# Performance work log

Measured on AMD Instinct MI355X. Metric: run time of the kernel, lower is better.

The kernel has to match this reference:

```python
import jax, jax.numpy as jnp
import numpy as np


def setup_inputs() -> dict:
    key = jax.random.key(0)
    k0, k1, k2, k3, k4, k5 = jax.random.split(key, 6)
    N, E, F, D, H = 50000, 1000000, 128, 32, 4
    # xavier_normal with gain = calculate_gain('relu') = sqrt(2)
    std = np.sqrt(2.0) * np.sqrt(2.0 / (F + D))
    return {
        "entity_features": jax.random.normal(k0, (N, 1, F), jnp.float32),
        "relation_features": jax.random.normal(k1, (E, 1, F), jnp.float32),
        "src": jax.random.randint(k2, (E,), 0, N, jnp.int32),
        "dst": jax.random.randint(k3, (E,), 0, N, jnp.int32),
        "w_q": jax.random.normal(k4, (H, F, D), jnp.float32) * std,
        "w_k": jax.random.normal(k5, (H, F, D), jnp.float32) * std,
    }


def reference(entity_features, relation_features, src, dst, w_q, w_k):
    # entity_features: (N, 1, F) -> repeat over heads is just a broadcast
    feat = entity_features[:, 0, :]        # (N, F)
    rel = relation_features[:, 0, :]       # (E, F)
    num_heads = w_q.shape[0]
    N = feat.shape[0]

    # per-head projections: q = feat @ w_q, k = feat @ w_k, erel = rel @ w_k
    q = jnp.einsum("nf,hfd->nhd", feat, w_q)      # (N, H, D)  'out_el'
    k = jnp.einsum("nf,hfd->nhd", feat, w_k)      # (N, H, D)  'out_er'
    erel = jnp.einsum("ef,hfd->ehd", rel, w_k)    # (E, H, D)  'out_erel'

    # v_dot_u: dst's out_er . src's out_el ; e_dot_u: edge out_erel . src's out_er
    e = (jnp.einsum("ehd,ehd->eh", k[dst], q[src])
         + jnp.einsum("ehd,ehd->eh", erel, k[src]))   # (E, H)
    e = jax.nn.leaky_relu(e, negative_slope=0.01)

    # edge_softmax normalized by source node (softmax over outgoing edges)
    m = jax.ops.segment_max(e, src, num_segments=N)   # (N, H)
    m = jnp.where(jnp.isfinite(m), m, jnp.zeros_like(m))
    ex = jnp.exp(e - m[src])                          # (E, H)
    denom = jax.ops.segment_sum(ex, src, num_segments=N)  # (N, H)
    att = ex / denom[src]                             # (E, H)

    # squeeze(-1).sum(-1)/num_heads on the (E, H, 1) edge tensor -> mean over heads
    return att.sum(axis=-1) / num_heads               # (E,)
```

## Files before the change

kernel.cpp:

```cpp
#include <hip/hip_runtime.h>

#define HH 4
#define FF 128
#define DD 32

typedef float f32x4 __attribute__((ext_vector_type(4)));


__global__ void scatter_kernel(const int* __restrict__ src, const int* __restrict__ dst,
                               int* __restrict__ cursor, int2* __restrict__ ed, int E) {
    int i = blockIdx.x * blockDim.x + threadIdx.x;
    if (i >= E) return;
    int s = src[i];
    int pos = atomicAdd(&cursor[s], 1);
    long long pack = (unsigned)i | ((long long)dst[i] << 32);
    __builtin_nontemporal_store(pack, (long long*)&ed[pos]);
}


__global__ __launch_bounds__(256) void qk_hist_kernel(
    const float* __restrict__ feat, const float* __restrict__ wq,
    const float* __restrict__ wk, float* __restrict__ q,
    float* __restrict__ k, int N,
    const int* __restrict__ src, int* __restrict__ counts, int E, int QKB) {
    __shared__ float fs[32 * FF];
    int bid = blockIdx.x;
    if (bid >= QKB) {
        int i = ((bid - QKB) * 256 + threadIdx.x) * 4;
        if (i + 3 < E) {
            int4 v = *(const int4*)(src + i);
            atomicAdd(&counts[v.x], 1);
            atomicAdd(&counts[v.y], 1);
            atomicAdd(&counts[v.z], 1);
            atomicAdd(&counts[v.w], 1);
        } else {
            for (; i < E; ++i) atomicAdd(&counts[src[i]], 1);
        }
        return;
    }
    int n0 = bid * 32;
    int nb = N - n0; if (nb > 32) nb = 32;
    const float4* s4 = (const float4*)(feat + (size_t)n0 * FF);
    int nf4 = nb * FF / 4;
    for (int i = threadIdx.x; i < nf4; i += 256) ((float4*)fs)[i] = s4[i];
    __syncthreads();

    int half = threadIdx.x >> 7;
    int o    = threadIdx.x & 127;
    int h = o >> 5, d = o & 31;
    const float* wqp = wq + ((size_t)h * FF) * DD + d;
    const float* wkp = wk + ((size_t)h * FF) * DD + d;

    float accq[16], acck[16];
#pragma unroll
    for (int e = 0; e < 16; ++e) { accq[e] = 0.f; acck[e] = 0.f; }
    for (int f = 0; f < FF; f += 4) {
        float wq0 = wqp[(f + 0) * DD], wq1 = wqp[(f + 1) * DD];
        float wq2 = wqp[(f + 2) * DD], wq3 = wqp[(f + 3) * DD];
        float wk0 = wkp[(f + 0) * DD], wk1 = wkp[(f + 1) * DD];
        float wk2 = wkp[(f + 2) * DD], wk3 = wkp[(f + 3) * DD];
#pragma unroll
        for (int e = 0; e < 16; ++e) {
            float4 fv = *(const float4*)&fs[(half * 16 + e) * FF + f];
            accq[e] += fv.x * wq0 + fv.y * wq1 + fv.z * wq2 + fv.w * wq3;
            acck[e] += fv.x * wk0 + fv.y * wk1 + fv.z * wk2 + fv.w * wk3;
        }
    }
    int ecnt = nb - half * 16; if (ecnt < 0) ecnt = 0; if (ecnt > 16) ecnt = 16;
    for (int e = 0; e < ecnt; ++e) {
        size_t n = (size_t)(n0 + half * 16 + e);
        q[(n * HH + h) * DD + d] = accq[e];
        k[(n * HH + h) * DD + d] = acck[e];
    }
}


__global__ __launch_bounds__(256) void kk_alloc_kernel(
    const float* __restrict__ kbuf, const float* __restrict__ wk,
    float* __restrict__ kkout, int N,
    const int* __restrict__ counts, int* __restrict__ startb,
    int* __restrict__ cursor, int* __restrict__ gcur, int KKB) {
    __shared__ float ks[16 * FF];
    int bid = blockIdx.x;
    if (bid >= KKB) {
        int sid = (bid - KKB) * 256 + threadIdx.x;
        int lane = threadIdx.x & 63;
        int cnt = (sid < N) ? counts[sid] : 0;
        int incl = cnt;
#pragma unroll
        for (int off = 1; off < 64; off <<= 1) {
            int y = __shfl_up(incl, off, 64);
            if (lane >= off) incl += y;
        }
        int total = __shfl(incl, 63, 64);
        int base = 0;
        if (lane == 63) base = atomicAdd(gcur, total);
        base = __shfl(base, 63, 64);
        if (sid < N) {
            int st = base + incl - cnt;
            startb[sid] = st;
            cursor[sid] = st;
        }
        return;
    }
    int n0 = bid * 16;
    int nb = N - n0; if (nb > 16) nb = 16;
    const float4* s4 = (const float4*)(kbuf + (size_t)n0 * FF);
    int nf4 = nb * FF / 4;
    for (int i = threadIdx.x; i < nf4; i += 256) ((float4*)ks)[i] = s4[i];
    __syncthreads();

    int o = threadIdx.x;
    int h1 = o >> 7, f1 = o & 127;
    int h2 = h1 + 2;
    const float* w1 = wk + ((size_t)h1 * FF + f1) * DD;
    const float* w2 = wk + ((size_t)h2 * FF + f1) * DD;

    float acc1[16], acc2[16];
#pragma unroll
    for (int e = 0; e < 16; ++e) { acc1[e] = 0.f; acc2[e] = 0.f; }
    for (int d = 0; d < DD; d += 4) {
        float4 wv1 = *(const float4*)&w1[d];
        float4 wv2 = *(const float4*)&w2[d];
#pragma unroll
        for (int e = 0; e < 16; ++e) {
            float4 k1 = *(const float4*)&ks[e * FF + h1 * DD + d];
            float4 k2 = *(const float4*)&ks[e * FF + h2 * DD + d];
            acc1[e] += k1.x * wv1.x + k1.y * wv1.y + k1.z * wv1.z + k1.w * wv1.w;
            acc2[e] += k2.x * wv2.x + k2.y * wv2.y + k2.z * wv2.z + k2.w * wv2.w;
        }
    }
    for (int e = 0; e < nb; ++e) {
        kkout[((size_t)(n0 + e) * HH + h1) * FF + f1] = acc1[e];
        kkout[((size_t)(n0 + e) * HH + h2) * FF + f1] = acc2[e];
    }
}


__device__ __forceinline__ int score4(
    const float* __restrict__ rel, const float* __restrict__ k,
    int pv, int dv, int j0, int g, int t,
    const float4* kkA, const float4* kkB, const float2* qv,
    float* ev, int* e_i_out) {
    int idx = j0 + g;
    int e_i = __shfl(pv, idx, 64);
    int dd  = __shfl(dv, idx, 64);
    *e_i_out = e_i;
    const float* rp = rel + (size_t)e_i * FF + t * 8;
    f32x4 r0 = __builtin_nontemporal_load((const f32x4*)rp);
    f32x4 r1 = __builtin_nontemporal_load((const f32x4*)(rp + 4));
#pragma unroll
    for (int h = 0; h < HH; ++h) {
        float2 kv = *(const float2*)(k + ((size_t)dd * HH + h) * DD + t * 2);
        float a = r0.x * kkA[h].x + r0.y * kkA[h].y + r0.z * kkA[h].z + r0.w * kkA[h].w
                + r1.x * kkB[h].x + r1.y * kkB[h].y + r1.z * kkB[h].z + r1.w * kkB[h].w
                + qv[h].x * kv.x + qv[h].y * kv.y;
#pragma unroll
        for (int off = 1; off < 16; off <<= 1) a += __shfl_xor(a, off, 64);
        ev[h] = a >= 0.f ? a : 0.01f * a;
    }
    return idx;
}

__global__ __launch_bounds__(256) void group_kernel(
    const float* __restrict__ rel, const int2* __restrict__ ed,
    const float* __restrict__ q, const float* __restrict__ k,
    const float* __restrict__ kk, const int* __restrict__ start,
    const int* __restrict__ counts, float* __restrict__ out, int N) {
    __shared__ __align__(16) float e_buf_all[4][128][4];
    int wid = threadIdx.x >> 6;
    int s = blockIdx.x * 4 + wid;
    if (s >= N) return;
    int cnt = counts[s];
    if (cnt == 0) return;
    int base = start[s];
    int lane = threadIdx.x & 63;
    int g = lane >> 4, t = lane & 15;
    int hsel = ((t & 1) << 1) | ((t & 2) >> 1);
    float (*e_buf)[4] = e_buf_all[wid];

    float4 kkA[HH], kkB[HH];
    float2 qv[HH];
    const float* kkbase = kk + (size_t)s * (HH * FF) + t * 8;
    const float* qbase  = q  + (size_t)s * (HH * DD) + t * 2;
#pragma unroll
    for (int h = 0; h < HH; ++h) {
        kkA[h] = *(const float4*)(kkbase + h * FF);
        kkB[h] = *(const float4*)(kkbase + h * FF + 4);
        qv[h]  = *(const float2*)(qbase + h * DD);
    }

    float mloc = -INFINITY;
    bool fast = (cnt <= 128);

    for (int c0 = 0; c0 < cnt; c0 += 64) {
        int nc = min(cnt - c0, 64);
        int pv = 0, dv = 0;
        if (lane < nc) { int2 pd = ed[base + c0 + lane]; pv = pd.x; dv = pd.y; }
        for (int j0 = 0; j0 < nc; j0 += 4) {
            int idx = j0 + g;
            int sel = idx < nc ? idx : 0;
            int e_i = __shfl(pv, sel, 64);
            int dd  = __shfl(dv, sel, 64);
            const float* rp = rel + (size_t)e_i * FF + t * 8;
            f32x4 r0 = __builtin_nontemporal_load((const f32x4*)rp);
            f32x4 r1 = __builtin_nontemporal_load((const f32x4*)(rp + 4));
            float p[HH];
#pragma unroll
            for (int h = 0; h < HH; ++h) {
                float2 kv = *(const float2*)(k + ((size_t)dd * HH + h) * DD + t * 2);
                p[h] = r0.x * kkA[h].x + r0.y * kkA[h].y + r0.z * kkA[h].z + r0.w * kkA[h].w
                     + r1.x * kkB[h].x + r1.y * kkB[h].y + r1.z * kkB[h].z + r1.w * kkB[h].w
                     + qv[h].x * kv.x + qv[h].y * kv.y;
            }
            float sx = (t & 1) ? p[0] : p[2];
            float sy = (t & 1) ? p[1] : p[3];
            float rx = __shfl_xor(sx, 1, 64);
            float ry = __shfl_xor(sy, 1, 64);
            float a0 = ((t & 1) ? p[2] : p[0]) + rx;
            float a1 = ((t & 1) ? p[3] : p[1]) + ry;
            float sz = (t & 2) ? a0 : a1;
            float rz = __shfl_xor(sz, 2, 64);
            float e = ((t & 2) ? a1 : a0) + rz;
            e += __shfl_xor(e, 4, 64);
            e += __shfl_xor(e, 8, 64);
            e = e >= 0.f ? e : 0.01f * e;
            if (idx < nc) {
                mloc = fmaxf(mloc, e);
                if (fast && t < 4) e_buf[c0 + idx][hsel] = e;
            }
        }
    }
    mloc = fmaxf(mloc, __shfl_xor(mloc, 16, 64));
    mloc = fmaxf(mloc, __shfl_xor(mloc, 32, 64));
    float m[HH];
    m[0] = __shfl(mloc, 0, 64);
    m[1] = __shfl(mloc, 2, 64);
    m[2] = __shfl(mloc, 1, 64);
    m[3] = __shfl(mloc, 3, 64);

    if (fast) {
        int i0 = lane, i1 = lane + 64;
        float ex0[HH] = {0.f, 0.f, 0.f, 0.f}, ex1[HH] = {0.f, 0.f, 0.f, 0.f};
        if (i0 < cnt) {
            float4 ev = *(const float4*)e_buf[i0];
            ex0[0] = __expf(ev.x - m[0]); ex0[1] = __expf(ev.y - m[1]);
            ex0[2] = __expf(ev.z - m[2]); ex0[3] = __expf(ev.w - m[3]);
        }
        if (i1 < cnt) {
            float4 ev = *(const float4*)e_buf[i1];
            ex1[0] = __expf(ev.x - m[0]); ex1[1] = __expf(ev.y - m[1]);
            ex1[2] = __expf(ev.z - m[2]); ex1[3] = __expf(ev.w - m[3]);
        }
        float rl[HH];
#pragma unroll
        for (int h = 0; h < HH; ++h) {
            float v = ex0[h] + ex1[h];
#pragma unroll
            for (int off = 1; off < 64; off <<= 1) v += __shfl_xor(v, off, 64);
            rl[h] = 1.0f / v;
        }
        if (i0 < cnt)
            out[ed[base + i0].x] = 0.25f * (ex0[0]*rl[0] + ex0[1]*rl[1] + ex0[2]*rl[2] + ex0[3]*rl[3]);
        if (i1 < cnt)
            out[ed[base + i1].x] = 0.25f * (ex1[0]*rl[0] + ex1[1]*rl[1] + ex1[2]*rl[2] + ex1[3]*rl[3]);
    } else {
        float lacc[HH] = {0.f, 0.f, 0.f, 0.f};
        for (int c0 = 0; c0 < cnt; c0 += 64) {
            int nc = min(cnt - c0, 64);
            int pv = 0, dv = 0;
            if (lane < nc) { int2 pd = ed[base + c0 + lane]; pv = pd.x; dv = pd.y; }
            for (int j0 = 0; j0 < nc; j0 += 4) {
                float ev[HH]; int e_i;
                int idx = score4(rel, k, pv, dv, j0, g, t, kkA, kkB, qv, ev, &e_i);
                if (idx < nc && t == 0) {
#pragma unroll
                    for (int h = 0; h < HH; ++h) lacc[h] += __expf(ev[h] - m[h]);
                }
            }
        }
        float rl[HH];
#pragma unroll
        for (int h = 0; h < HH; ++h) {
            float v = lacc[h];
#pragma unroll
            for (int off = 1; off < 64; off <<= 1) v += __shfl_xor(v, off, 64);
            rl[h] = 1.0f / v;
        }
        for (int c0 = 0; c0 < cnt; c0 += 64) {
            int nc = min(cnt - c0, 64);
            int pv = 0, dv = 0;
            if (lane < nc) { int2 pd = ed[base + c0 + lane]; pv = pd.x; dv = pd.y; }
            for (int j0 = 0; j0 < nc; j0 += 4) {
                float ev[HH]; int e_i;
                int idx = score4(rel, k, pv, dv, j0, g, t, kkA, kkB, qv, ev, &e_i);
                if (idx < nc && t == 0) {
                    float a = __expf(ev[0]-m[0])*rl[0] + __expf(ev[1]-m[1])*rl[1]
                            + __expf(ev[2]-m[2])*rl[2] + __expf(ev[3]-m[3])*rl[3];
                    out[e_i] = 0.25f * a;
                }
            }
        }
    }
}

extern "C" void kernel_launch(void* const* d_in, const int* in_sizes, int n_in,
                              void* d_out, int out_size, void* d_ws, size_t ws_size,
                              hipStream_t stream) {
    const float* feat = (const float*)d_in[0];
    const float* rel  = (const float*)d_in[1];
    const int*   src  = (const int*)d_in[2];
    const int*   dst  = (const int*)d_in[3];
    const float* wq   = (const float*)d_in[4];
    const float* wk   = (const float*)d_in[5];
    float* out = (float*)d_out;

    const int N = in_sizes[0] / FF;
    const int E = in_sizes[2];

    float* q      = (float*)d_ws;
    float* k      = q  + (size_t)N * HH * DD;
    float* kk     = k  + (size_t)N * HH * DD;
    int*   counts = (int*)(kk + (size_t)N * HH * FF);
    int*   gcur   = counts + N;
    int*   start  = gcur + 1;
    int*   cursor = start + N;
    int2*  ed     = (int2*)(cursor + N);

    int nb  = (N + 255) / 256;
    int QKB = (N + 31) / 32;
    int HB  = (E + 1023) / 1024;
    int KKB = (N + 15) / 16;

    hipMemsetAsync(counts, 0, (size_t)(N + 1) * sizeof(int), stream);
    qk_hist_kernel<<<QKB + HB, 256, 0, stream>>>(feat, wq, wk, q, k, N, src, counts, E, QKB);
    kk_alloc_kernel<<<KKB + nb, 256, 0, stream>>>(k, wk, kk, N, counts, start, cursor, gcur, KKB);
    scatter_kernel<<<(E + 255) / 256, 256, 0, stream>>>(src, dst, cursor, ed, E);
    group_kernel<<<(N + 3) / 4, 256, 0, stream>>>(rel, ed, q, k, kk, start, counts, out, N);
}
```

Baseline: 419.4 us.

## Permute relation features into source-sorted order during scatter

The scatter kernel now copies each edge's relation feature row into a workspace buffer at its source-grouped position, one 16-lane group per edge. The group kernel then reads relation rows contiguously by sorted position instead of gathering them by original edge index. This makes the group kernel's reads sequential, but it adds a full extra read and scattered write of the large relation tensor plus a large workspace allocation.

```diff
diff --git a/kernel.cpp b/kernel.cpp
--- a/kernel.cpp
+++ b/kernel.cpp
@@ -7,14 +7,28 @@
 typedef float f32x4 __attribute__((ext_vector_type(4)));
 
 
-__global__ void scatter_kernel(const int* __restrict__ src, const int* __restrict__ dst,
-                               int* __restrict__ cursor, int2* __restrict__ ed, int E) {
-    int i = blockIdx.x * blockDim.x + threadIdx.x;
-    if (i >= E) return;
-    int s = src[i];
-    int pos = atomicAdd(&cursor[s], 1);
-    long long pack = (unsigned)i | ((long long)dst[i] << 32);
-    __builtin_nontemporal_store(pack, (long long*)&ed[pos]);
+__global__ __launch_bounds__(256) void scatter_kernel(
+    const int* __restrict__ src, const int* __restrict__ dst,
+    const float* __restrict__ rel, int* __restrict__ cursor,
+    int2* __restrict__ ed, float* __restrict__ rel_s, int E) {
+    int tid = threadIdx.x;
+    int e = blockIdx.x * 16 + (tid >> 4);
+    if (e >= E) return;
+    int u = tid & 15;
+    int pos = 0;
+    if (u == 0) {
+        pos = atomicAdd(&cursor[src[e]], 1);
+        long long pack = (unsigned)e | ((long long)dst[e] << 32);
+        __builtin_nontemporal_store(pack, (long long*)&ed[pos]);
+    }
+    int lane = tid & 63;
+    pos = __shfl(pos, lane & ~15, 64);
+    const f32x4* rp = (const f32x4*)(rel + (size_t)e * FF + u * 8);
+    f32x4 a = __builtin_nontemporal_load(rp);
+    f32x4 b = __builtin_nontemporal_load(rp + 1);
+    f32x4* wp = (f32x4*)(rel_s + (size_t)pos * FF + u * 8);
+    __builtin_nontemporal_store(a, wp);
+    __builtin_nontemporal_store(b, wp + 1);
 }
 
 
@@ -137,16 +151,11 @@
 }
 
 
-__device__ __forceinline__ int score4(
-    const float* __restrict__ rel, const float* __restrict__ k,
-    int pv, int dv, int j0, int g, int t,
-    const float4* kkA, const float4* kkB, const float2* qv,
-    float* ev, int* e_i_out) {
-    int idx = j0 + g;
-    int e_i = __shfl(pv, idx, 64);
-    int dd  = __shfl(dv, idx, 64);
-    *e_i_out = e_i;
-    const float* rp = rel + (size_t)e_i * FF + t * 8;
+__device__ __forceinline__ void score_row(
+    const float* __restrict__ rel_s, const float* __restrict__ k,
+    int row, int dd, int t,
+    const float4* kkA, const float4* kkB, const float2* qv, float* ev) {
+    const float* rp = rel_s + (size_t)row * FF + t * 8;
     f32x4 r0 = __builtin_nontemporal_load((const f32x4*)rp);
     f32x4 r1 = __builtin_nontemporal_load((const f32x4*)(rp + 4));
 #pragma unroll
@@ -159,11 +168,10 @@
         for (int off = 1; off < 16; off <<= 1) a += __shfl_xor(a, off, 64);
         ev[h] = a >= 0.f ? a : 0.01f * a;
     }
-    return idx;
 }
 
 __global__ __launch_bounds__(256) void group_kernel(
-    const float* __restrict__ rel, const int2* __restrict__ ed,
+    const float* __restrict__ rel_s, const int2* __restrict__ ed,
     const float* __restrict__ q, const float* __restrict__ k,
     const float* __restrict__ kk, const int* __restrict__ start,
     const int* __restrict__ counts, float* __restrict__ out, int N) {
@@ -195,14 +203,13 @@
 
     for (int c0 = 0; c0 < cnt; c0 += 64) {
         int nc = min(cnt - c0, 64);
-        int pv = 0, dv = 0;
-        if (lane < nc) { int2 pd = ed[base + c0 + lane]; pv = pd.x; dv = pd.y; }
+        int dv = 0;
+        if (lane < nc) dv = ed[base + c0 + lane].y;
         for (int j0 = 0; j0 < nc; j0 += 4) {
             int idx = j0 + g;
             int sel = idx < nc ? idx : 0;
-            int e_i = __shfl(pv, sel, 64);
             int dd  = __shfl(dv, sel, 64);
-            const float* rp = rel + (size_t)e_i * FF + t * 8;
+            const float* rp = rel_s + (size_t)(base + c0 + sel) * FF + t * 8;
             f32x4 r0 = __builtin_nontemporal_load((const f32x4*)rp);
             f32x4 r1 = __builtin_nontemporal_load((const f32x4*)(rp + 4));
             float p[HH];
@@ -268,11 +275,14 @@
         float lacc[HH] = {0.f, 0.f, 0.f, 0.f};
         for (int c0 = 0; c0 < cnt; c0 += 64) {
             int nc = min(cnt - c0, 64);
-            int pv = 0, dv = 0;
-            if (lane < nc) { int2 pd = ed[base + c0 + lane]; pv = pd.x; dv = pd.y; }
+            int dv = 0;
+            if (lane < nc) dv = ed[base + c0 + lane].y;
             for (int j0 = 0; j0 < nc; j0 += 4) {
-                float ev[HH]; int e_i;
-                int idx = score4(rel, k, pv, dv, j0, g, t, kkA, kkB, qv, ev, &e_i);
+                int idx = j0 + g;
+                int sel = idx < nc ? idx : 0;
+                int dd  = __shfl(dv, sel, 64);
+                float ev[HH];
+                score_row(rel_s, k, base + c0 + sel, dd, t, kkA, kkB, qv, ev);
                 if (idx < nc && t == 0) {
 #pragma unroll
                     for (int h = 0; h < HH; ++h) lacc[h] += __expf(ev[h] - m[h]);
@@ -292,8 +302,12 @@
             int pv = 0, dv = 0;
             if (lane < nc) { int2 pd = ed[base + c0 + lane]; pv = pd.x; dv = pd.y; }
             for (int j0 = 0; j0 < nc; j0 += 4) {
-                float ev[HH]; int e_i;
-                int idx = score4(rel, k, pv, dv, j0, g, t, kkA, kkB, qv, ev, &e_i);
+                int idx = j0 + g;
+                int sel = idx < nc ? idx : 0;
+                int e_i = __shfl(pv, sel, 64);
+                int dd  = __shfl(dv, sel, 64);
+                float ev[HH];
+                score_row(rel_s, k, base + c0 + sel, dd, t, kkA, kkB, qv, ev);
                 if (idx < nc && t == 0) {
                     float a = __expf(ev[0]-m[0])*rl[0] + __expf(ev[1]-m[1])*rl[1]
                             + __expf(ev[2]-m[2])*rl[2] + __expf(ev[3]-m[3])*rl[3];
@@ -318,12 +332,13 @@
     const int N = in_sizes[0] / FF;
     const int E = in_sizes[2];
 
-    float* q      = (float*)d_ws;
+    float* rel_s  = (float*)d_ws;
+    float* q      = rel_s + (size_t)E * FF;
     float* k      = q  + (size_t)N * HH * DD;
     float* kk     = k  + (size_t)N * HH * DD;
     int*   counts = (int*)(kk + (size_t)N * HH * FF);
     int*   gcur   = counts + N;
-    int*   start  = gcur + 1;
+    int*   start  = gcur + 2;
     int*   cursor = start + N;
     int2*  ed     = (int2*)(cursor + N);
 
@@ -332,9 +347,9 @@
     int HB  = (E + 1023) / 1024;
     int KKB = (N + 15) / 16;
 
-    hipMemsetAsync(counts, 0, (size_t)(N + 1) * sizeof(int), stream);
+    hipMemsetAsync(counts, 0, (size_t)(N + 2) * sizeof(int), stream);
     qk_hist_kernel<<<QKB + HB, 256, 0, stream>>>(feat, wq, wk, q, k, N, src, counts, E, QKB);
     kk_alloc_kernel<<<KKB + nb, 256, 0, stream>>>(k, wk, kk, N, counts, start, cursor, gcur, KKB);
-    scatter_kernel<<<(E + 255) / 256, 256, 0, stream>>>(src, dst, cursor, ed, E);
-    group_kernel<<<(N + 3) / 4, 256, 0, stream>>>(rel, ed, q, k, kk, start, counts, out, N);
-}
+    scatter_kernel<<<(E + 15) / 16, 256, 0, stream>>>(src, dst, rel, cursor, ed, rel_s, E);
+    group_kernel<<<(N + 3) / 4, 256, 0, stream>>>(rel_s, ed, q, k, kk, start, counts, out, N);
+}
```

New measurement: 612.2 us. 1.46x slower.
